# Kernel optimization log

Hardware: AMD Instinct MI355X
Metric: run time of the kernel (lower is better)

Reference implementation:

```python
import jax, jax.numpy as jnp
import numpy as np

B, C, H, W = 4, 64, 192, 192
G = 8           # offset groups per input stream
OFF_CH = 27 * G # 216 channels in each offset input
MAG = 10.0
KH = KW = 3
PAD = 1


def setup_inputs() -> dict:
    key = jax.random.key(0)
    ks = jax.random.split(key, 7)
    rn = lambda k, s, sc=1.0: jax.random.normal(k, s, dtype=jnp.float32) * sc
    return {
        "x1": rn(ks[0], (B, C, H, W)),
        "offset1": rn(ks[1], (B, OFF_CH, H, W)),
        "flow1": rn(ks[2], (B, 2, H, W), 2.0),
        "x2": rn(ks[3], (B, C, H, W)),
        "offset2": rn(ks[4], (B, OFF_CH, H, W)),
        "flow2": rn(ks[5], (B, 2, H, W), 2.0),
        "weight": rn(ks[6], (C, (2 * C) // (2 * G), KH, KW), 0.05),  # groups = 16
        "bias": jnp.zeros((C,), jnp.float32),
    }


def _prep(out, flow, magnitude):
    # chunk into (o1, o2, mask) along channels
    o1, o2, m = jnp.split(out, 3, axis=1)
    mask = jax.nn.sigmoid(m)
    off = jnp.tanh(jnp.concatenate([o1, o2], axis=1)) * magnitude
    rep = off.shape[1] // 2
    # flow.flip(1).repeat(1, rep, 1, 1) -> tile the 2-channel (fy, fx) pattern
    off = off + jnp.tile(flow[:, ::-1], (1, rep, 1, 1))
    return off, mask


def _deform_conv(x, offset, mask, weight, bias):
    # x: [B, Cin, H, W]; offset: [B, 2*n_off*9, H, W]; mask: [B, n_off*9, H, W]
    b, cin, h, w = x.shape
    n_off = 2 * G                      # 16 offset groups == 16 weight groups
    cg = cin // n_off                  # channels per group (8)
    K = KH * KW
    off = offset.reshape(b, n_off, K, 2, h, w)
    m = mask.reshape(b, n_off, K, h, w)
    k = jnp.arange(K)
    ki = (k // KW).astype(x.dtype)
    kj = (k % KW).astype(x.dtype)
    ys = jnp.arange(h, dtype=x.dtype)
    xs = jnp.arange(w, dtype=x.dtype)
    # sampling positions [B, n_off, K, H, W]; (dy, dx) channel order as torchvision
    py = off[:, :, :, 0] + ki[None, None, :, None, None] + (ys - PAD)[None, None, None, :, None]
    px = off[:, :, :, 1] + kj[None, None, :, None, None] + (xs - PAD)[None, None, None, None, :]
    y0 = jnp.floor(py)
    x0 = jnp.floor(px)
    wy = py - y0
    wx = px - x0
    x_r = x.reshape(b, n_off, cg, h * w)
    val = jnp.zeros((b, n_off, cg, K, h, w), x.dtype)
    # bilinear gather, zero outside image (4 fixed corners)
    corners = [(y0, x0, (1 - wy) * (1 - wx)), (y0, x0 + 1, (1 - wy) * wx),
               (y0 + 1, x0, wy * (1 - wx)), (y0 + 1, x0 + 1, wy * wx)]
    for yc, xc, wgt in corners:
        valid = ((yc >= 0) & (yc <= h - 1) & (xc >= 0) & (xc <= w - 1)).astype(x.dtype)
        yi = jnp.clip(yc, 0, h - 1).astype(jnp.int32)
        xi = jnp.clip(xc, 0, w - 1).astype(jnp.int32)
        idx = (yi * w + xi).reshape(b, n_off, 1, K * h * w)
        gat = jnp.take_along_axis(x_r, idx, axis=3).reshape(b, n_off, cg, K, h, w)
        val = val + gat * (wgt * valid)[:, :, None]
    val = val * m[:, :, None]          # modulation
    cout = weight.shape[0]
    og = cout // n_off                 # out channels per group (4)
    w_r = weight.reshape(n_off, og, cg, K)
    out = jnp.einsum('bgckhw,gock->bgohw', val, w_r).reshape(b, cout, h, w)
    return out + bias[None, :, None, None]


def reference(x1, offset1, flow1, x2, offset2, flow2, weight, bias):
    o1, m1 = _prep(offset1, flow1, MAG)
    o2, m2 = _prep(offset2, flow2, MAG)
    x = jnp.concatenate([x1, x2], axis=1)
    off = jnp.concatenate([o1, o2], axis=1)
    msk = jnp.concatenate([m1, m2], axis=1)
    return _deform_conv(x, off, msk, weight, bias)
```

## Files before the change

### kernel.cpp

```cpp
#include <hip/hip_runtime.h>

#define H 192
#define W 192
#define HW (192 * 192)

typedef _Float16 half2_t __attribute__((ext_vector_type(2)));

__device__ __forceinline__ float frcp(float x) { return __builtin_amdgcn_rcpf(x); }
__device__ __forceinline__ float ftanh(float x) {
    float t = __expf(x * 2.0f);
    return 1.0f - 2.0f * frcp(t + 1.0f);
}
__device__ __forceinline__ float fsigmoid(float x) {
    return frcp(1.0f + __expf(-x));
}
__device__ __forceinline__ half2_t splat(float v) {
    _Float16 h = (_Float16)v;
    half2_t r = {h, h};
    return r;
}

__global__ __launch_bounds__(256)
void transpose_x(const float* __restrict__ x1, const float* __restrict__ x2,
                 uint4* __restrict__ xt)
{
    const int pix = blockIdx.x * 256 + threadIdx.x;
    const int bg  = blockIdx.y;
    const int b = bg >> 4, gg = bg & 15;
    const int s = gg >> 3, g = gg & 7;
    const float* xb = (s ? x2 : x1) + (size_t)(b * 64 + g * 8) * HW + pix;
    unsigned w0[4];
#pragma unroll
    for (int j = 0; j < 4; ++j) {
        half2_t h = {(_Float16)xb[(size_t)(2 * j) * HW],
                     (_Float16)xb[(size_t)(2 * j + 1) * HW]};
        w0[j] = __builtin_bit_cast(unsigned, h);
    }
    xt[(size_t)bg * HW + pix] = make_uint4(w0[0], w0[1], w0[2], w0[3]);
}

__global__ __launch_bounds__(256)
void dcn_gather(const float* __restrict__ off1, const float* __restrict__ flow1,
                const float* __restrict__ off2, const float* __restrict__ flow2,
                const float* __restrict__ wgt, const float* __restrict__ bias,
                const uint4* __restrict__ xt, float* __restrict__ out)
{
    const int tile = blockIdx.x;
    const int gg   = blockIdx.y;
    const int b    = blockIdx.z;
    const int tilex = tile % 6, tiley = tile / 6;
    const int lx = threadIdx.x & 31, ly = threadIdx.x >> 5;
    const int x = tilex * 32 + lx;
    const int y = tiley * 8 + ly;
    const int pix = y * W + x;

    __shared__ half2_t wsh2[9][4][4];
    for (int i = threadIdx.x; i < 144; i += 256) {
        const int k = i >> 4, r = i & 15, j = r >> 2, o = r & 3;
        const float lo = wgt[gg * 288 + o * 72 + (2 * j) * 9 + k];
        const float hi = wgt[gg * 288 + o * 72 + (2 * j + 1) * 9 + k];
        wsh2[k][j][o] = half2_t{(_Float16)lo, (_Float16)hi};
    }
    __syncthreads();

    const int s = gg >> 3;
    const int g = gg & 7;
    const float* ob = (s ? off2 : off1) + (size_t)b * 216 * HW + pix;
    const float* fb = (s ? flow2 : flow1) + (size_t)b * 2 * HW + pix;
    const uint4* tb = xt + (size_t)(b * 16 + gg) * HW;

    float rdy[9], rdx[9], rm[9];
#pragma unroll
    for (int k = 0; k < 9; ++k) {
        const int t = g * 9 + k;
        rdy[k] = ob[(size_t)(2 * t) * HW];
        rdx[k] = ob[(size_t)(2 * t + 1) * HW];
        rm[k]  = ob[(size_t)(144 + t) * HW];
    }
    const float f0 = fb[0];
    const float f1 = fb[HW];

    int     idc[9][4];
    half2_t hw00[9], hw01[9], hw10[9], hw11[9];
#pragma unroll
    for (int k = 0; k < 9; ++k) {
        const float mk = fsigmoid(rm[k]);
        const float py = ftanh(rdy[k]) * 10.0f + f1 + (float)(k / 3 + y - 1);
        const float px = ftanh(rdx[k]) * 10.0f + f0 + (float)(k % 3 + x - 1);
        const float fy0 = floorf(py);
        const float fx0 = floorf(px);
        const float wy = py - fy0;
        const float wx = px - fx0;
        const int y0 = (int)fy0, x0 = (int)fx0;
        const int y1 = y0 + 1, x1i = x0 + 1;
        const bool vy0 = (unsigned)y0  < (unsigned)H;
        const bool vy1 = (unsigned)y1  < (unsigned)H;
        const bool vx0 = (unsigned)x0  < (unsigned)W;
        const bool vx1 = (unsigned)x1i < (unsigned)W;
        float w00 = (1.0f - wy) * (1.0f - wx) * mk;
        float w01 = (1.0f - wy) * wx * mk;
        float w10 = wy * (1.0f - wx) * mk;
        float w11 = wy * wx * mk;
        hw00[k] = splat((vy0 && vx0) ? w00 : 0.0f);
        hw01[k] = splat((vy0 && vx1) ? w01 : 0.0f);
        hw10[k] = splat((vy1 && vx0) ? w10 : 0.0f);
        hw11[k] = splat((vy1 && vx1) ? w11 : 0.0f);
        const int iy0 = min(max(y0, 0), H - 1);
        const int iy1 = min(max(y1, 0), H - 1);
        const int ix0 = min(max(x0, 0), W - 1);
        const int ix1 = min(max(x1i, 0), W - 1);
        idc[k][0] = iy0 * W + ix0;
        idc[k][1] = iy0 * W + ix1;
        idc[k][2] = iy1 * W + ix0;
        idc[k][3] = iy1 * W + ix1;
    }

    float acc0 = bias[gg * 4 + 0];
    float acc1 = bias[gg * 4 + 1];
    float acc2 = bias[gg * 4 + 2];
    float acc3 = bias[gg * 4 + 3];

#pragma unroll
    for (int k = 0; k < 9; ++k) {
        const uint4 q00 = tb[idc[k][0]];
        const uint4 q01 = tb[idc[k][1]];
        const uint4 q10 = tb[idc[k][2]];
        const uint4 q11 = tb[idc[k][3]];
        const half2_t* A = (const half2_t*)&q00;
        const half2_t* Bq = (const half2_t*)&q01;
        const half2_t* Cq = (const half2_t*)&q10;
        const half2_t* Dq = (const half2_t*)&q11;
#pragma unroll
        for (int j = 0; j < 4; ++j) {
            half2_t vb = hw00[k] * A[j];
            vb = hw01[k] * Bq[j] + vb;
            vb = hw10[k] * Cq[j] + vb;
            vb = hw11[k] * Dq[j] + vb;
            half2_t w0 = wsh2[k][j][0];
            half2_t w1 = wsh2[k][j][1];
            half2_t w2 = wsh2[k][j][2];
            half2_t w3 = wsh2[k][j][3];
            acc0 = __builtin_amdgcn_fdot2(vb, w0, acc0, false);
            acc1 = __builtin_amdgcn_fdot2(vb, w1, acc1, false);
            acc2 = __builtin_amdgcn_fdot2(vb, w2, acc2, false);
            acc3 = __builtin_amdgcn_fdot2(vb, w3, acc3, false);
        }
    }

    float* op = out + ((size_t)(b * 64 + gg * 4)) * HW + pix;
    op[0 * HW] = acc0;
    op[1 * HW] = acc1;
    op[2 * HW] = acc2;
    op[3 * HW] = acc3;
}

__global__ __launch_bounds__(256)
void dcn_fused(const float* __restrict__ x1, const float* __restrict__ off1,
               const float* __restrict__ flow1, const float* __restrict__ x2,
               const float* __restrict__ off2, const float* __restrict__ flow2,
               const float* __restrict__ wgt, const float* __restrict__ bias,
               float* __restrict__ out)
{
    const int tile = blockIdx.x;
    const int gg   = blockIdx.y;
    const int b    = blockIdx.z;
    const int tilex = tile % 6, tiley = tile / 6;
    const int lx = threadIdx.x & 31, ly = threadIdx.x >> 5;
    const int x = tilex * 32 + lx;
    const int y = tiley * 8 + ly;
    const int pix = y * W + x;

    __shared__ float wsh[9][8][4];
    for (int i = threadIdx.x; i < 288; i += 256) {
        int o = i / 72;
        int r = i - o * 72;
        int c = r / 9;
        int k = r - c * 9;
        wsh[k][c][o] = wgt[gg * 288 + i];
    }
    __syncthreads();

    const int s = gg >> 3;
    const int g = gg & 7;
    const float* xb = (s ? x2 : x1) + (size_t)(b * 64 + g * 8) * HW;
    const float* ob = (s ? off2 : off1) + (size_t)b * 216 * HW;
    const float* fb = (s ? flow2 : flow1) + (size_t)b * 2 * HW;

    const float f0 = fb[pix];
    const float f1 = fb[HW + pix];

    float acc0 = bias[gg * 4 + 0];
    float acc1 = bias[gg * 4 + 1];
    float acc2 = bias[gg * 4 + 2];
    float acc3 = bias[gg * 4 + 3];

    for (int k = 0; k < 9; ++k) {
        const int t = g * 9 + k;
        const float rdy = ob[(size_t)(2 * t) * HW + pix];
        const float rdx = ob[(size_t)(2 * t + 1) * HW + pix];
        const float rm  = ob[(size_t)(144 + t) * HW + pix];
        const float mk = fsigmoid(rm);
        const float py = ftanh(rdy) * 10.0f + f1 + (float)(k / 3 + y - 1);
        const float px = ftanh(rdx) * 10.0f + f0 + (float)(k % 3 + x - 1);
        const float fy0 = floorf(py);
        const float fx0 = floorf(px);
        const float wy = py - fy0;
        const float wx = px - fx0;
        const int y0 = (int)fy0, x0 = (int)fx0;
        const int y1 = y0 + 1, x1i = x0 + 1;
        const bool vy0 = (unsigned)y0  < (unsigned)H;
        const bool vy1 = (unsigned)y1  < (unsigned)H;
        const bool vx0 = (unsigned)x0  < (unsigned)W;
        const bool vx1 = (unsigned)x1i < (unsigned)W;
        float w00 = (1.0f - wy) * (1.0f - wx) * mk;
        float w01 = (1.0f - wy) * wx * mk;
        float w10 = wy * (1.0f - wx) * mk;
        float w11 = wy * wx * mk;
        w00 = (vy0 && vx0) ? w00 : 0.0f;
        w01 = (vy0 && vx1) ? w01 : 0.0f;
        w10 = (vy1 && vx0) ? w10 : 0.0f;
        w11 = (vy1 && vx1) ? w11 : 0.0f;
        const int iy0 = min(max(y0, 0), H - 1);
        const int iy1 = min(max(y1, 0), H - 1);
        const int ix0 = min(max(x0, 0), W - 1);
        const int ix1 = min(max(x1i, 0), W - 1);
        const int o00 = iy0 * W + ix0;
        const int o01 = iy0 * W + ix1;
        const int o10 = iy1 * W + ix0;
        const int o11 = iy1 * W + ix1;
#pragma unroll
        for (int c = 0; c < 8; ++c) {
            const float* p = xb + (size_t)c * HW;
            const float v = p[o00] * w00 + p[o01] * w01 + p[o10] * w10 + p[o11] * w11;
            acc0 = fmaf(wsh[k][c][0], v, acc0);
            acc1 = fmaf(wsh[k][c][1], v, acc1);
            acc2 = fmaf(wsh[k][c][2], v, acc2);
            acc3 = fmaf(wsh[k][c][3], v, acc3);
        }
    }

    float* op = out + ((size_t)(b * 64 + gg * 4)) * HW + pix;
    op[0 * HW] = acc0;
    op[1 * HW] = acc1;
    op[2 * HW] = acc2;
    op[3 * HW] = acc3;
}

extern "C" void kernel_launch(void* const* d_in, const int* in_sizes, int n_in,
                              void* d_out, int out_size, void* d_ws, size_t ws_size,
                              hipStream_t stream) {
    const float* x1    = (const float*)d_in[0];
    const float* off1  = (const float*)d_in[1];
    const float* flow1 = (const float*)d_in[2];
    const float* x2    = (const float*)d_in[3];
    const float* off2  = (const float*)d_in[4];
    const float* flow2 = (const float*)d_in[5];
    const float* wgt   = (const float*)d_in[6];
    const float* bias  = (const float*)d_in[7];
    float* out = (float*)d_out;

    const size_t need = (size_t)4 * 16 * HW * 8 * 2;
    if (ws_size >= need) {
        uint4* xt = (uint4*)d_ws;
        transpose_x<<<dim3(HW / 256, 64, 1), 256, 0, stream>>>(x1, x2, xt);
        dcn_gather<<<dim3(144, 16, 4), 256, 0, stream>>>(off1, flow1, off2, flow2,
                                                         wgt, bias, xt, out);
    } else {
        dcn_fused<<<dim3(144, 16, 4), 256, 0, stream>>>(x1, off1, flow1, x2, off2,
                                                        flow2, wgt, bias, out);
    }
}
```

Measured before the change: 204.5 us.

## Stage a haloed input window in LDS for deformable bilinear gathers

The deformable-conv gather kernel is replaced by one that processes 32x16 pixel tiles with 512 threads. Each block first cooperatively loads a halo-21 window of the fp16-packed input into shared memory. The four bilinear corner reads per tap then come from LDS, with a global-memory fallback only when a sample falls outside the window and still has nonzero weight. Block indices are also swizzled across tiles. The aim is to replace scattered global/L2 gathers with coalesced bulk loads plus LDS reads. In exchange, the roughly 68 KB shared-memory footprint limits blocks per CU, and there is a divergent fallback path.

```diff
diff --git a/kernel.cpp b/kernel.cpp
--- a/kernel.cpp
+++ b/kernel.cpp
@@ -3,6 +3,12 @@
 #define H 192
 #define W 192
 #define HW (192 * 192)
+
+#define TX 32
+#define TY 16
+#define HALO 21
+#define WC (TX + 2 * HALO)
+#define WR (TY + 2 * HALO)
 
 typedef _Float16 half2_t __attribute__((ext_vector_type(2)));
 
@@ -39,24 +45,39 @@
     xt[(size_t)bg * HW + pix] = make_uint4(w0[0], w0[1], w0[2], w0[3]);
 }
 
-__global__ __launch_bounds__(256)
-void dcn_gather(const float* __restrict__ off1, const float* __restrict__ flow1,
-                const float* __restrict__ off2, const float* __restrict__ flow2,
-                const float* __restrict__ wgt, const float* __restrict__ bias,
-                const uint4* __restrict__ xt, float* __restrict__ out)
+__global__ __launch_bounds__(512, 4)
+void dcn_lds(const float* __restrict__ off1, const float* __restrict__ flow1,
+             const float* __restrict__ off2, const float* __restrict__ flow2,
+             const float* __restrict__ wgt, const float* __restrict__ bias,
+             const uint4* __restrict__ xt, float* __restrict__ out)
 {
-    const int tile = blockIdx.x;
-    const int gg   = blockIdx.y;
-    const int b    = blockIdx.z;
+    __shared__ uint4 win[WR * WC];
+    __shared__ half2_t wsh2[9][4][4];
+
+    const int t_raw = blockIdx.x;
+    const int tile  = (t_raw & 7) * 9 + (t_raw >> 3);
+    const int gg = blockIdx.y;
+    const int b  = blockIdx.z;
     const int tilex = tile % 6, tiley = tile / 6;
-    const int lx = threadIdx.x & 31, ly = threadIdx.x >> 5;
-    const int x = tilex * 32 + lx;
-    const int y = tiley * 8 + ly;
+    const int X0 = tilex * TX, Y0 = tiley * TY;
+    const int tid = threadIdx.x;
+    const int lx = tid & 31, ly = tid >> 5;
+    const int x = X0 + lx, y = Y0 + ly;
     const int pix = y * W + x;
 
-    __shared__ half2_t wsh2[9][4][4];
-    for (int i = threadIdx.x; i < 144; i += 256) {
-        const int k = i >> 4, r = i & 15, j = r >> 2, o = r & 3;
+    const uint4* tb = xt + (size_t)(b * 16 + gg) * HW;
+    const int wy0 = Y0 - HALO, wx0 = X0 - HALO;
+
+    for (int i = tid; i < WR * WC; i += 512) {
+        const int r = i / WC, c = i - r * WC;
+        const int gy = wy0 + r, gx = wx0 + c;
+        uint4 v = make_uint4(0, 0, 0, 0);
+        if ((unsigned)gy < (unsigned)H && (unsigned)gx < (unsigned)W)
+            v = tb[gy * W + gx];
+        win[i] = v;
+    }
+    if (tid < 144) {
+        const int k = tid >> 4, r = tid & 15, j = r >> 2, o = r & 3;
         const float lo = wgt[gg * 288 + o * 72 + (2 * j) * 9 + k];
         const float hi = wgt[gg * 288 + o * 72 + (2 * j + 1) * 9 + k];
         wsh2[k][j][o] = half2_t{(_Float16)lo, (_Float16)hi};
@@ -67,7 +88,6 @@
     const int g = gg & 7;
     const float* ob = (s ? off2 : off1) + (size_t)b * 216 * HW + pix;
     const float* fb = (s ? flow2 : flow1) + (size_t)b * 2 * HW + pix;
-    const uint4* tb = xt + (size_t)(b * 16 + gg) * HW;
 
     float rdy[9], rdx[9], rm[9];
 #pragma unroll
@@ -80,7 +100,9 @@
     const float f0 = fb[0];
     const float f1 = fb[HW];
 
-    int     idc[9][4];
+    int     l00a[9];
+    int     lyx[9];
+    int     fbm = 0;
     half2_t hw00[9], hw01[9], hw10[9], hw11[9];
 #pragma unroll
     for (int k = 0; k < 9; ++k) {
@@ -92,27 +114,28 @@
         const float wy = py - fy0;
         const float wx = px - fx0;
         const int y0 = (int)fy0, x0 = (int)fx0;
-        const int y1 = y0 + 1, x1i = x0 + 1;
-        const bool vy0 = (unsigned)y0  < (unsigned)H;
-        const bool vy1 = (unsigned)y1  < (unsigned)H;
-        const bool vx0 = (unsigned)x0  < (unsigned)W;
-        const bool vx1 = (unsigned)x1i < (unsigned)W;
-        float w00 = (1.0f - wy) * (1.0f - wx) * mk;
-        float w01 = (1.0f - wy) * wx * mk;
-        float w10 = wy * (1.0f - wx) * mk;
-        float w11 = wy * wx * mk;
-        hw00[k] = splat((vy0 && vx0) ? w00 : 0.0f);
-        hw01[k] = splat((vy0 && vx1) ? w01 : 0.0f);
-        hw10[k] = splat((vy1 && vx0) ? w10 : 0.0f);
-        hw11[k] = splat((vy1 && vx1) ? w11 : 0.0f);
-        const int iy0 = min(max(y0, 0), H - 1);
-        const int iy1 = min(max(y1, 0), H - 1);
-        const int ix0 = min(max(x0, 0), W - 1);
-        const int ix1 = min(max(x1i, 0), W - 1);
-        idc[k][0] = iy0 * W + ix0;
-        idc[k][1] = iy0 * W + ix1;
-        idc[k][2] = iy1 * W + ix0;
-        idc[k][3] = iy1 * W + ix1;
+        const bool vy0 = (unsigned)y0       < (unsigned)H;
+        const bool vy1 = (unsigned)(y0 + 1) < (unsigned)H;
+        const bool vx0 = (unsigned)x0       < (unsigned)W;
+        const bool vx1 = (unsigned)(x0 + 1) < (unsigned)W;
+        const float w00 = (vy0 && vx0) ? (1.0f - wy) * (1.0f - wx) * mk : 0.0f;
+        const float w01 = (vy0 && vx1) ? (1.0f - wy) * wx * mk : 0.0f;
+        const float w10 = (vy1 && vx0) ? wy * (1.0f - wx) * mk : 0.0f;
+        const float w11 = (vy1 && vx1) ? wy * wx * mk : 0.0f;
+        hw00[k] = splat(w00);
+        hw01[k] = splat(w01);
+        hw10[k] = splat(w10);
+        hw11[k] = splat(w11);
+
+        const int ly0 = y0 - wy0;
+        const int lx0 = x0 - wx0;
+        const bool okwin = ((unsigned)ly0 <= (unsigned)(WR - 2)) &&
+                           ((unsigned)lx0 <= (unsigned)(WC - 2));
+        const bool anyw = (w00 + w01 + w10 + w11) > 0.0f;
+        const bool needfb = (!okwin) && anyw;
+        fbm |= needfb ? (1 << k) : 0;
+        l00a[k] = okwin ? (ly0 * WC + lx0) : 0;
+        lyx[k] = (lx0 & 0xffff) | (ly0 << 16);
     }
 
     float acc0 = bias[gg * 4 + 0];
@@ -122,11 +145,25 @@
 
 #pragma unroll
     for (int k = 0; k < 9; ++k) {
-        const uint4 q00 = tb[idc[k][0]];
-        const uint4 q01 = tb[idc[k][1]];
-        const uint4 q10 = tb[idc[k][2]];
-        const uint4 q11 = tb[idc[k][3]];
-        const half2_t* A = (const half2_t*)&q00;
+        const int base = l00a[k];
+        uint4 q00 = win[base];
+        uint4 q01 = win[base + 1];
+        uint4 q10 = win[base + WC];
+        uint4 q11 = win[base + WC + 1];
+        if ((fbm >> k) & 1) {
+            const int lx0v = (int)(short)(lyx[k] & 0xffff);
+            const int ly0v = (int)(short)((unsigned)lyx[k] >> 16);
+            const int ay0 = wy0 + ly0v, ax0 = wx0 + lx0v;
+            const int iy0 = min(max(ay0, 0), H - 1);
+            const int iy1 = min(max(ay0 + 1, 0), H - 1);
+            const int ix0 = min(max(ax0, 0), W - 1);
+            const int ix1 = min(max(ax0 + 1, 0), W - 1);
+            q00 = tb[iy0 * W + ix0];
+            q01 = tb[iy0 * W + ix1];
+            q10 = tb[iy1 * W + ix0];
+            q11 = tb[iy1 * W + ix1];
+        }
+        const half2_t* A  = (const half2_t*)&q00;
         const half2_t* Bq = (const half2_t*)&q01;
         const half2_t* Cq = (const half2_t*)&q10;
         const half2_t* Dq = (const half2_t*)&q11;
@@ -263,8 +300,8 @@
     if (ws_size >= need) {
         uint4* xt = (uint4*)d_ws;
         transpose_x<<<dim3(HW / 256, 64, 1), 256, 0, stream>>>(x1, x2, xt);
-        dcn_gather<<<dim3(144, 16, 4), 256, 0, stream>>>(off1, flow1, off2, flow2,
-                                                         wgt, bias, xt, out);
+        dcn_lds<<<dim3(72, 16, 4), 512, 0, stream>>>(off1, flow1, off2, flow2,
+                                                     wgt, bias, xt, out);
     } else {
         dcn_fused<<<dim3(144, 16, 4), 256, 0, stream>>>(x1, off1, flow1, x2, off2,
                                                         flow2, wgt, bias, out);
```

After: 743.0 us. 263% more time.
